# Kernel tuning notes

Measured on AMD Instinct MI355X. Metric: run time of the kernel, lower is better.

The kernel has to match this reference:

```python
import jax, jax.numpy as jnp
import numpy as np

B, N, F, U, S = 64, 4096, 2, 16, 2


def setup_inputs() -> dict:
    key = jax.random.key(0)
    ks = jax.random.split(key, 7)
    inputs = jax.random.normal(ks[0], (B, F * N), dtype=jnp.float32)
    state = jax.random.normal(ks[1], (B, U * N), dtype=jnp.float32)

    def random_walk(k):
        a = jax.random.uniform(k, (N, N), dtype=jnp.float32)
        return a / jnp.sum(a, axis=1, keepdims=True)  # row-stochastic like D^-1 A

    support0 = random_walk(ks[2])
    support1 = random_walk(ks[3])
    kshape = ((F + U) * S, U)
    scale = jnp.float32(1.0 / np.sqrt(kshape[0]))
    r_kernel = jax.random.normal(ks[4], kshape, dtype=jnp.float32) * scale
    u_kernel = jax.random.normal(ks[5], kshape, dtype=jnp.float32) * scale
    c_kernel = jax.random.normal(ks[6], kshape, dtype=jnp.float32) * scale
    return {"inputs": inputs, "state": state, "support0": support0,
            "support1": support1, "r_kernel": r_kernel, "u_kernel": u_kernel,
            "c_kernel": c_kernel}


def _diffuse(x, supports):
    # x: (B, C, N); K.dot(x, support.T)[b,c,m] = sum_n x[b,c,n] * support[m,n]
    return jnp.concatenate([jnp.einsum('bcn,mn->bcm', x, s) for s in supports], axis=1)


def reference(inputs, state, support0, support1, r_kernel, u_kernel, c_kernel):
    supports = (support0, support1)
    feats = inputs.reshape(B, F, N)
    prev = state.reshape(B, U, N)

    h = _diffuse(feats, supports).transpose(0, 2, 1)   # (B, N, S*F)
    st = _diffuse(prev, supports).transpose(0, 2, 1)   # (B, N, S*U)
    hs = jnp.concatenate([h, st], axis=-1)             # (B, N, S*(F+U))

    r = jax.nn.sigmoid(hs @ r_kernel)                  # (B, N, U)
    u = jax.nn.sigmoid(hs @ u_kernel)                  # (B, N, U)

    prev_t = prev.transpose(0, 2, 1)                   # (B, N, U)
    r_prev = (r * prev_t).transpose(0, 2, 1)           # (B, U, N)
    c_state = _diffuse(r_prev, supports).transpose(0, 2, 1)  # (B, N, S*U)
    c = jnp.tanh(jnp.concatenate([h, c_state], axis=-1) @ c_kernel)  # (B, N, U)

    z = u * prev_t + (1.0 - u) * c                     # (B, N, U)
    # original: activation=None -> linear, then K.reshape(output, (-1, units*num_nodes))
    return z.reshape(B, U * N)
```

## Files before the change

kernel.cpp:

```cpp
#include <hip/hip_runtime.h>
#include <cstdint>

#define KDIM 4096
#define NNODE 4096
#define KSPLIT 2
#define TSTEPS 128
#define THALF (TSTEPS / KSPLIT)

typedef __bf16 bf16x8 __attribute__((ext_vector_type(8)));
typedef float floatx4 __attribute__((ext_vector_type(4)));

__device__ __forceinline__ uint16_t f2b(float f) {
  union { float f; uint32_t u; } v; v.f = f;
  uint32_t u = v.u;
  return (uint16_t)((u + 0x7FFFu + ((u >> 16) & 1u)) >> 16);
}
__device__ __forceinline__ float b2f(uint16_t h) {
  union { uint32_t u; float f; } v; v.u = ((uint32_t)h) << 16; return v.f;
}
__device__ __forceinline__ uint32_t pack2(float a, float b) {
  return (uint32_t)f2b(a) | ((uint32_t)f2b(b) << 16);
}


__global__ __launch_bounds__(256) void cvt_supports(
    const float* __restrict__ s0, const float* __restrict__ s1,
    uint16_t* __restrict__ d0, uint16_t* __restrict__ d1) {
  const float* src = blockIdx.z ? s1 : s0;
  uint16_t* dst = blockIdx.z ? d1 : d0;
  const int c16 = blockIdx.x, kb = blockIdx.y;
  const int col_in = threadIdx.x >> 4, k8 = threadIdx.x & 15;
  const int col = c16 * 16 + col_in;
  const int k = kb * 128 + k8 * 8;
  const float* p = src + (size_t)col * KDIM + k;
  float4 v0 = *(const float4*)p;
  float4 v1 = *(const float4*)(p + 4);
  uint4 o;
  o.x = pack2(v0.x, v0.y); o.y = pack2(v0.z, v0.w);
  o.z = pack2(v1.x, v1.y); o.w = pack2(v1.z, v1.w);
  size_t off = ((size_t)(c16 * 128 + kb * 4 + (k8 >> 2))) * 512 +
               (size_t)((k8 & 3) * 16 + col_in) * 8;
  *(uint4*)(dst + off) = o;
}

__global__ __launch_bounds__(256) void pack_x1(
    const float* __restrict__ inp, const float* __restrict__ st,
    uint16_t* __restrict__ X1) {
  const int r16 = blockIdx.x, kb = blockIdx.y;
  const int row_in = threadIdx.x >> 4, k8 = threadIdx.x & 15;
  const int row = r16 * 16 + row_in;
  const int k = kb * 128 + k8 * 8;
  int b = row / 18, c = row - b * 18;
  const float* p = (c < 2) ? (inp + (size_t)b * 8192 + (size_t)c * 4096 + k)
                           : (st + (size_t)b * 65536 + (size_t)(c - 2) * 4096 + k);
  float4 v0 = *(const float4*)p;
  float4 v1 = *(const float4*)(p + 4);
  uint4 o;
  o.x = pack2(v0.x, v0.y); o.y = pack2(v0.z, v0.w);
  o.z = pack2(v1.x, v1.y); o.w = pack2(v1.z, v1.w);
  size_t off = ((size_t)(r16 * 128 + kb * 4 + (k8 >> 2))) * 512 +
               (size_t)((k8 & 3) * 16 + row_in) * 8;
  *(uint4*)(X1 + off) = o;
}

__device__ __forceinline__ void gl_lds16(const uint16_t* g, uint16_t* l) {
  __builtin_amdgcn_global_load_lds(
      (const __attribute__((address_space(1))) uint32_t*)g,
      (__attribute__((address_space(3))) uint32_t*)l, 16, 0, 0);
}

template <int MODE>
__global__ __launch_bounds__(256, 2) void gemm_frag(
    const uint16_t* __restrict__ Af, const uint16_t* __restrict__ S0f,
    const uint16_t* __restrict__ S1f, uint16_t* __restrict__ D) {
  constexpr int CPB = (MODE == 1) ? 18 : 16;
  constexpr int OUTC = (MODE == 1) ? 36 : 32;
  constexpr size_t PSTRIDE = (size_t)64 * OUTC * NNODE;
  constexpr int NCH = THALF;

  __shared__ uint16_t sAB[4][16][512];

  const int lane = threadIdx.x & 63, wave = threadIdx.x >> 6;
  const int wr = wave >> 1, wc = wave & 1;
  const int s = blockIdx.z & 1, ks = blockIdx.z >> 1;
  const uint16_t* __restrict__ Bf = s ? S1f : S0f;
  const int yF = blockIdx.y * 8;
  const int xF = blockIdx.x * 8;
  const int tBeg = ks * THALF;

  const bool isB = wave >= 2;
  const int fbase = (wave & 1) * 4;
  const uint16_t* Gw = (isB ? Bf : Af) +
      ((size_t)((isB ? xF : yF) + fbase) * 128 + (size_t)tBeg) * 512 +
      (size_t)lane * 8;
  const int slotw = (isB ? 8 : 0) + fbase;

  floatx4 acc[4][4];
#pragma unroll
  for (int i = 0; i < 4; ++i)
#pragma unroll
    for (int j = 0; j < 4; ++j) acc[i][j] = (floatx4){0.f, 0.f, 0.f, 0.f};

  auto STAGE = [&](int bi, int c) {
    const uint16_t* gt = Gw + (size_t)c * 512;
#pragma unroll
    for (int i = 0; i < 4; ++i)
      gl_lds16(gt + (size_t)i * 65536, &sAB[bi][slotw + i][0]);
  };

  auto LDREG = [&](int bi, bf16x8* a, bf16x8* b) {
#pragma unroll
    for (int rt = 0; rt < 4; ++rt)
      a[rt] = *(const bf16x8*)&sAB[bi][wr * 4 + rt][lane * 8];
#pragma unroll
    for (int ct = 0; ct < 4; ++ct)
      b[ct] = *(const bf16x8*)&sAB[bi][8 + wc * 4 + ct][lane * 8];
  };

  auto MFMA16 = [&](bf16x8* a, bf16x8* b) {
    __builtin_amdgcn_s_setprio(1);
#pragma unroll
    for (int rt = 0; rt < 4; ++rt)
#pragma unroll
      for (int ct = 0; ct < 4; ++ct)
        acc[rt][ct] = __builtin_amdgcn_mfma_f32_16x16x32_bf16(
            a[rt], b[ct], acc[rt][ct], 0, 0, 0);
    __builtin_amdgcn_s_setprio(0);
  };

  STAGE(0, 0);
  STAGE(1, 1);
  STAGE(2, 2);
  asm volatile("s_waitcnt vmcnt(8)" ::: "memory");
  __builtin_amdgcn_sched_barrier(0);
  __builtin_amdgcn_s_barrier();
  __builtin_amdgcn_sched_barrier(0);
  bf16x8 aA[4], bA[4], aB[4], bB[4];
  LDREG(0, aA, bA);

#define GEMM_ITER(J, RDBUF, STBUF, CURA, CURB, NXTA, NXTB)                  \
  {                                                                         \
    int cl = c0 + 3 + (J);                                                  \
    if (cl > NCH - 1) cl = NCH - 1;       \
    STAGE((STBUF), cl);                                                     \
    asm volatile("s_waitcnt vmcnt(8)" ::: "memory");                        \
    __builtin_amdgcn_sched_barrier(0);                                      \
    __builtin_amdgcn_s_barrier();                                           \
    __builtin_amdgcn_sched_barrier(0);                                      \
    LDREG((RDBUF), NXTA, NXTB);                                             \
    asm volatile("s_waitcnt lgkmcnt(8)" ::: "memory");                      \
    __builtin_amdgcn_sched_barrier(0);                                      \
    MFMA16(CURA, CURB);                                                     \
    __builtin_amdgcn_sched_barrier(0);                                      \
  }

  for (int m = 0; m < NCH / 4; ++m) {
    const int c0 = m * 4;
    GEMM_ITER(0, 1, 3, aA, bA, aB, bB)
    GEMM_ITER(1, 2, 0, aB, bB, aA, bA)
    GEMM_ITER(2, 3, 1, aA, bA, aB, bB)
    GEMM_ITER(3, 0, 2, aB, bB, aA, bA)
  }
#undef GEMM_ITER

  uint16_t* Dp = D + (size_t)ks * PSTRIDE;
#pragma unroll
  for (int rt = 0; rt < 4; ++rt) {
#pragma unroll
    for (int r = 0; r < 4; ++r) {
      int rowg = yF * 16 + wr * 64 + rt * 16 + (lane >> 4) * 4 + r;
      int b = rowg / CPB, c = rowg - b * CPB;
      int jj;
      if (MODE == 1) jj = (c < 2) ? (2 * s + c) : (4 + 16 * s + (c - 2));
      else jj = 16 * s + c;
      uint16_t* drow = Dp + (size_t)(b * OUTC + jj) * NNODE;
#pragma unroll
      for (int ct = 0; ct < 4; ++ct) {
        int colg = xF * 16 + wc * 64 + ct * 16 + (lane & 15);
        drow[colg] = f2b(acc[rt][ct][r]);
      }
    }
  }
}

__global__ __launch_bounds__(256) void stage2(
    const uint16_t* __restrict__ P1, const float* __restrict__ state,
    const float* __restrict__ rk, const float* __restrict__ uk,
    uint16_t* __restrict__ X2f, float* __restrict__ U) {
  constexpr size_t PS = (size_t)64 * 36 * NNODE;
  __shared__ float s_rk[576], s_uk[576];
  __shared__ uint16_t s_x2[16 * 264];
  for (int i = threadIdx.x; i < 576; i += 256) { s_rk[i] = rk[i]; s_uk[i] = uk[i]; }
  __syncthreads();
  const int b = blockIdx.x >> 4, nb = blockIdx.x & 15;
  const int i = threadIdx.x;
  const int n = nb * 256 + i;
  float hs[36];
  const uint16_t* p = P1 + (size_t)b * 36 * NNODE + n;
#pragma unroll
  for (int j = 0; j < 36; ++j)
    hs[j] = b2f(p[(size_t)j * NNODE]) + b2f(p[PS + (size_t)j * NNODE]);
  float ar[16], au[16];
#pragma unroll
  for (int k = 0; k < 16; ++k) { ar[k] = 0.f; au[k] = 0.f; }
#pragma unroll
  for (int j = 0; j < 36; ++j) {
    float h = hs[j];
#pragma unroll
    for (int k = 0; k < 16; ++k) {
      ar[k] += h * s_rk[j * 16 + k];
      au[k] += h * s_uk[j * 16 + k];
    }
  }
  const float* sp = state + (size_t)b * 65536 + n;
#pragma unroll
  for (int k = 0; k < 16; ++k) {
    float r = 1.f / (1.f + __expf(-ar[k]));
    float uu = 1.f / (1.f + __expf(-au[k]));
    float prev = sp[(size_t)k * NNODE];
    s_x2[k * 264 + i] = f2b(r * prev);
    U[(size_t)(b * 16 + k) * NNODE + n] = uu;
  }
  __syncthreads();
  uint16_t* region = X2f + ((size_t)b * 128 + nb * 8) * 512;
#pragma unroll
  for (int rr = 0; rr < 2; ++rr) {
    int fid = rr * 256 + i;
    int kk = fid & 15, qq = (fid >> 4) & 3, tl = fid >> 6;
    uint4 v = *(const uint4*)&s_x2[kk * 264 + tl * 32 + qq * 8];
    *(uint4*)(region + (size_t)fid * 8) = v;
  }
}

__global__ __launch_bounds__(256) void stage4(
    const uint16_t* __restrict__ P1, const uint16_t* __restrict__ P3,
    const float* __restrict__ U, const float* __restrict__ state,
    const float* __restrict__ ck, float* __restrict__ out) {
  constexpr size_t PS1 = (size_t)64 * 36 * NNODE;
  constexpr size_t PS3 = (size_t)64 * 32 * NNODE;
  __shared__ float s_ck[576];
  for (int i = threadIdx.x; i < 576; i += 256) s_ck[i] = ck[i];
  __syncthreads();
  int idx = blockIdx.x * 256 + threadIdx.x;
  int b = idx >> 12, n = idx & 4095;
  float hv[36];
  const uint16_t* p1 = P1 + (size_t)b * 36 * NNODE + n;
#pragma unroll
  for (int j = 0; j < 4; ++j)
    hv[j] = b2f(p1[(size_t)j * NNODE]) + b2f(p1[PS1 + (size_t)j * NNODE]);
  const uint16_t* p3 = P3 + (size_t)b * 32 * NNODE + n;
#pragma unroll
  for (int j = 0; j < 32; ++j)
    hv[4 + j] = b2f(p3[(size_t)j * NNODE]) + b2f(p3[PS3 + (size_t)j * NNODE]);
  float ac[16];
#pragma unroll
  for (int k = 0; k < 16; ++k) ac[k] = 0.f;
#pragma unroll
  for (int j = 0; j < 36; ++j) {
    float h = hv[j];
#pragma unroll
    for (int k = 0; k < 16; ++k) ac[k] += h * s_ck[j * 16 + k];
  }
  const float* sp = state + (size_t)b * 65536 + n;
  const float* up = U + (size_t)b * 16 * NNODE + n;
  float z[16];
#pragma unroll
  for (int k = 0; k < 16; ++k) {
    float e = __expf(2.f * ac[k]);
    float c = 1.f - 2.f / (e + 1.f);
    float uu = up[(size_t)k * NNODE];
    float prev = sp[(size_t)k * NNODE];
    z[k] = uu * prev + (1.f - uu) * c;
  }
  float4* po = (float4*)(out + (size_t)b * 65536 + (size_t)n * 16);
#pragma unroll
  for (int k4 = 0; k4 < 4; ++k4)
    po[k4] = make_float4(z[k4 * 4], z[k4 * 4 + 1], z[k4 * 4 + 2], z[k4 * 4 + 3]);
}

extern "C" void kernel_launch(void* const* d_in, const int* in_sizes, int n_in,
                              void* d_out, int out_size, void* d_ws, size_t ws_size,
                              hipStream_t stream) {
  const float* inputs = (const float*)d_in[0];
  const float* state = (const float*)d_in[1];
  const float* s0 = (const float*)d_in[2];
  const float* s1 = (const float*)d_in[3];
  const float* rk = (const float*)d_in[4];
  const float* uk = (const float*)d_in[5];
  const float* ck = (const float*)d_in[6];
  float* out = (float*)d_out;
  char* ws = (char*)d_ws;

  uint16_t* S0f = (uint16_t*)(ws);
  uint16_t* S1f = (uint16_t*)(ws + 33554432);
  uint16_t* X1f = (uint16_t*)(ws + 67108864);
  uint16_t* X2f = (uint16_t*)(ws + 67108864);
  uint16_t* P1 = (uint16_t*)(ws + 76546048);
  float* U = (float*)(ws + 114294784);
  uint16_t* P3 = (uint16_t*)(ws + 131072000);

  cvt_supports<<<dim3(256, 32, 2), 256, 0, stream>>>(s0, s1, S0f, S1f);
  pack_x1<<<dim3(72, 32), 256, 0, stream>>>(inputs, state, X1f);
  gemm_frag<1><<<dim3(32, 9, 2 * KSPLIT), 256, 0, stream>>>(X1f, S0f, S1f, P1);
  stage2<<<1024, 256, 0, stream>>>(P1, state, rk, uk, X2f, U);
  gemm_frag<3><<<dim3(32, 8, 2 * KSPLIT), 256, 0, stream>>>(X2f, S0f, S1f, P3);
  stage4<<<1024, 256, 0, stream>>>(P1, P3, U, state, ck, out);
}
```

Baseline: 352.5 us.

## Widen GEMM block tile to 128x256 with triple-buffered LDS staging

The fragment GEMM now gives each block twice as many B (support) columns, so every wave holds a 4x8 grid of MFMA accumulators instead of 4x4. Staging is reorganised so each wave loads six fragments per chunk into a 3-deep LDS ring, replacing the 4-deep ring with 16 slots. The grid's x dimension is halved to match. The aim is to reuse each A fragment across more columns and reduce redundant A loads and L2 traffic, at the cost of more accumulator registers, a shallower prefetch pipeline and half as many blocks.

```diff
diff --git a/kernel.cpp b/kernel.cpp
--- a/kernel.cpp
+++ b/kernel.cpp
@@ -78,51 +78,56 @@
   constexpr size_t PSTRIDE = (size_t)64 * OUTC * NNODE;
   constexpr int NCH = THALF;
 
-  __shared__ uint16_t sAB[4][16][512];
+  __shared__ uint16_t sAB[3][24][512];
 
   const int lane = threadIdx.x & 63, wave = threadIdx.x >> 6;
   const int wr = wave >> 1, wc = wave & 1;
   const int s = blockIdx.z & 1, ks = blockIdx.z >> 1;
   const uint16_t* __restrict__ Bf = s ? S1f : S0f;
   const int yF = blockIdx.y * 8;
-  const int xF = blockIdx.x * 8;
+  const int xF = blockIdx.x * 16;
   const int tBeg = ks * THALF;
 
-  const bool isB = wave >= 2;
-  const int fbase = (wave & 1) * 4;
-  const uint16_t* Gw = (isB ? Bf : Af) +
-      ((size_t)((isB ? xF : yF) + fbase) * 128 + (size_t)tBeg) * 512 +
-      (size_t)lane * 8;
-  const int slotw = (isB ? 8 : 0) + fbase;
-
-  floatx4 acc[4][4];
+  const uint16_t* Gp[6];
+#pragma unroll
+  for (int i = 0; i < 6; ++i) {
+    int fid = wave * 6 + i;
+    bool isA = fid < 8;
+    int fr = isA ? (yF + fid) : (xF + fid - 8);
+    const uint16_t* base = isA ? Af : Bf;
+    Gp[i] = base + ((size_t)fr * 128 + tBeg) * 512 + (size_t)lane * 8;
+  }
+
+  floatx4 acc[4][8];
 #pragma unroll
   for (int i = 0; i < 4; ++i)
 #pragma unroll
-    for (int j = 0; j < 4; ++j) acc[i][j] = (floatx4){0.f, 0.f, 0.f, 0.f};
+    for (int j = 0; j < 8; ++j) acc[i][j] = (floatx4){0.f, 0.f, 0.f, 0.f};
 
   auto STAGE = [&](int bi, int c) {
-    const uint16_t* gt = Gw + (size_t)c * 512;
-#pragma unroll
-    for (int i = 0; i < 4; ++i)
-      gl_lds16(gt + (size_t)i * 65536, &sAB[bi][slotw + i][0]);
+    uint16_t* l = &sAB[bi][wave * 6][0];
+    const size_t off = (size_t)c * 512;
+#pragma unroll
+    for (int i = 0; i < 6; ++i)
+      gl_lds16(Gp[i] + off, l + (size_t)i * 512);
   };
 
   auto LDREG = [&](int bi, bf16x8* a, bf16x8* b) {
+    const uint16_t* base = &sAB[bi][0][lane * 8];
 #pragma unroll
     for (int rt = 0; rt < 4; ++rt)
-      a[rt] = *(const bf16x8*)&sAB[bi][wr * 4 + rt][lane * 8];
-#pragma unroll
-    for (int ct = 0; ct < 4; ++ct)
-      b[ct] = *(const bf16x8*)&sAB[bi][8 + wc * 4 + ct][lane * 8];
+      a[rt] = *(const bf16x8*)(base + (size_t)(wr * 4 + rt) * 512);
+#pragma unroll
+    for (int ct = 0; ct < 8; ++ct)
+      b[ct] = *(const bf16x8*)(base + (size_t)(8 + wc * 8 + ct) * 512);
   };
 
-  auto MFMA16 = [&](bf16x8* a, bf16x8* b) {
+  auto MFMA32 = [&](bf16x8* a, bf16x8* b) {
     __builtin_amdgcn_s_setprio(1);
 #pragma unroll
     for (int rt = 0; rt < 4; ++rt)
 #pragma unroll
-      for (int ct = 0; ct < 4; ++ct)
+      for (int ct = 0; ct < 8; ++ct)
         acc[rt][ct] = __builtin_amdgcn_mfma_f32_16x16x32_bf16(
             a[rt], b[ct], acc[rt][ct], 0, 0, 0);
     __builtin_amdgcn_s_setprio(0);
@@ -130,36 +135,35 @@
 
   STAGE(0, 0);
   STAGE(1, 1);
-  STAGE(2, 2);
-  asm volatile("s_waitcnt vmcnt(8)" ::: "memory");
+  asm volatile("s_waitcnt vmcnt(6)" ::: "memory");
   __builtin_amdgcn_sched_barrier(0);
   __builtin_amdgcn_s_barrier();
   __builtin_amdgcn_sched_barrier(0);
-  bf16x8 aA[4], bA[4], aB[4], bB[4];
+  bf16x8 aA[4], bA[8], aB[4], bB[8];
   LDREG(0, aA, bA);
 
-#define GEMM_ITER(J, RDBUF, STBUF, CURA, CURB, NXTA, NXTB)                  \
+  int bN = 1, bS = 2;
+#define GEMM_ITER(CC, CURA, CURB, NXTA, NXTB)                               \
   {                                                                         \
-    int cl = c0 + 3 + (J);                                                  \
+    int cl = (CC) + 2;                                                      \
     if (cl > NCH - 1) cl = NCH - 1;       \
-    STAGE((STBUF), cl);                                                     \
-    asm volatile("s_waitcnt vmcnt(8)" ::: "memory");                        \
+    STAGE(bS, cl);                                                          \
+    asm volatile("s_waitcnt vmcnt(6)" ::: "memory");                        \
     __builtin_amdgcn_sched_barrier(0);                                      \
     __builtin_amdgcn_s_barrier();                                           \
     __builtin_amdgcn_sched_barrier(0);                                      \
-    LDREG((RDBUF), NXTA, NXTB);                                             \
-    asm volatile("s_waitcnt lgkmcnt(8)" ::: "memory");                      \
+    LDREG(bN, NXTA, NXTB);                                                  \
+    asm volatile("s_waitcnt lgkmcnt(12)" ::: "memory");                     \
     __builtin_amdgcn_sched_barrier(0);                                      \
-    MFMA16(CURA, CURB);                                                     \
+    MFMA32(CURA, CURB);                                                     \
     __builtin_amdgcn_sched_barrier(0);                                      \
-  }
-
-  for (int m = 0; m < NCH / 4; ++m) {
-    const int c0 = m * 4;
-    GEMM_ITER(0, 1, 3, aA, bA, aB, bB)
-    GEMM_ITER(1, 2, 0, aB, bB, aA, bA)
-    GEMM_ITER(2, 3, 1, aA, bA, aB, bB)
-    GEMM_ITER(3, 0, 2, aB, bB, aA, bA)
+    bN = (bN == 2) ? 0 : bN + 1;                                            \
+    bS = (bS == 2) ? 0 : bS + 1;                                            \
+  }
+
+  for (int c = 0; c < NCH; c += 2) {
+    GEMM_ITER(c,     aA, bA, aB, bB)
+    GEMM_ITER(c + 1, aB, bB, aA, bA)
   }
 #undef GEMM_ITER
 
@@ -175,8 +179,8 @@
       else jj = 16 * s + c;
       uint16_t* drow = Dp + (size_t)(b * OUTC + jj) * NNODE;
 #pragma unroll
-      for (int ct = 0; ct < 4; ++ct) {
-        int colg = xF * 16 + wc * 64 + ct * 16 + (lane & 15);
+      for (int ct = 0; ct < 8; ++ct) {
+        int colg = xF * 16 + wc * 128 + ct * 16 + (lane & 15);
         drow[colg] = f2b(acc[rt][ct][r]);
       }
     }
@@ -301,8 +305,8 @@
 
   cvt_supports<<<dim3(256, 32, 2), 256, 0, stream>>>(s0, s1, S0f, S1f);
   pack_x1<<<dim3(72, 32), 256, 0, stream>>>(inputs, state, X1f);
-  gemm_frag<1><<<dim3(32, 9, 2 * KSPLIT), 256, 0, stream>>>(X1f, S0f, S1f, P1);
+  gemm_frag<1><<<dim3(16, 9, 2 * KSPLIT), 256, 0, stream>>>(X1f, S0f, S1f, P1);
   stage2<<<1024, 256, 0, stream>>>(P1, state, rk, uk, X2f, U);
-  gemm_frag<3><<<dim3(32, 8, 2 * KSPLIT), 256, 0, stream>>>(X2f, S0f, S1f, P3);
+  gemm_frag<3><<<dim3(16, 8, 2 * KSPLIT), 256, 0, stream>>>(X2f, S0f, S1f, P3);
   stage4<<<1024, 256, 0, stream>>>(P1, P3, U, state, ck, out);
 }
```

After: 364.5 us. 1.03x slower.
